# Optimization experiments

Hardware: AMD Instinct MI355X
Metric: run time of the kernel (lower is better)

Reference implementation:

```python
import jax, jax.numpy as jnp
import numpy as np
from jax import lax

B, IMG = 2, 512
FMC, HID, A, NC = 1024, 512, 9, 21
RED, POOL, TOP, IOU_THR = 16, 7, 20, 0.3
NEG = -1e30
# 3 scales x 3 aspect ratios (w, h)
ANCHOR_WH = np.array([[s * np.sqrt(r), s / np.sqrt(r)] for s in (64.0, 128.0, 256.0) for r in (0.5, 1.0, 2.0)], dtype=np.float32)


def conv(x, w, b, stride, pad):
    y = lax.conv_general_dilated(x, w, (stride, stride), pad, dimension_numbers=('NCHW', 'OIHW', 'NCHW'))
    return y + b[None, :, None, None]


def make_anchors(H, W, stride):
    cy = (jnp.arange(H, dtype=jnp.float32) + 0.5) * stride
    cx = (jnp.arange(W, dtype=jnp.float32) + 0.5) * stride
    cyg, cxg = jnp.meshgrid(cy, cx, indexing='ij')  # [H,W]
    wh = jnp.asarray(ANCHOR_WH)  # [A,2]
    w2 = wh[None, None, :, 0] / 2
    h2 = wh[None, None, :, 1] / 2
    cxg = cxg[:, :, None]
    cyg = cyg[:, :, None]
    boxes = jnp.stack([cxg - w2, cyg - h2, cxg + w2, cyg + h2], axis=-1)  # [H,W,A,4]
    return boxes.reshape(-1, 4)


def box_iou(b, boxes):
    # b [4], boxes [N,4], (x1,y1,x2,y2)
    ix1 = jnp.maximum(b[0], boxes[:, 0])
    iy1 = jnp.maximum(b[1], boxes[:, 1])
    ix2 = jnp.minimum(b[2], boxes[:, 2])
    iy2 = jnp.minimum(b[3], boxes[:, 3])
    inter = jnp.maximum(ix2 - ix1, 0.0) * jnp.maximum(iy2 - iy1, 0.0)
    ab = jnp.maximum(b[2] - b[0], 0.0) * jnp.maximum(b[3] - b[1], 0.0)
    ar = jnp.maximum(boxes[:, 2] - boxes[:, 0], 0.0) * jnp.maximum(boxes[:, 3] - boxes[:, 1], 0.0)
    return inter / (ab + ar - inter + 1e-8)


def nms_one(boxes, scores):
    # greedy NMS, fixed TOP selections
    n = scores.shape[0]
    idxs = jnp.arange(n)

    def step(s, _):
        i = jnp.argmax(s)
        b, sc = boxes[i], s[i]
        s = jnp.where((box_iou(b, boxes) > IOU_THR) | (idxs == i), NEG, s)
        return s, (b, sc)

    _, (bs, ss) = lax.scan(step, scores, None, length=TOP)
    return bs, ss  # [TOP,4], [TOP]


def roi_align_one(fm_b, boxes):
    # fm_b [C,H,W], boxes [R,4] in image coords -> [R,C,POOL,POOL]
    C, H, W = fm_b.shape
    b = boxes / RED
    t = (jnp.arange(POOL, dtype=jnp.float32) + 0.5) / POOL
    xs = b[:, 0:1] + jnp.maximum(b[:, 2] - b[:, 0], 0.0)[:, None] * t[None]  # [R,P]
    ys = b[:, 1:2] + jnp.maximum(b[:, 3] - b[:, 1], 0.0)[:, None] * t[None]
    x = jnp.clip(xs[:, None, :], 0.0, W - 1.0) * jnp.ones((1, POOL, 1), jnp.float32)  # [R,P,P]
    y = jnp.clip(ys[:, :, None], 0.0, H - 1.0) * jnp.ones((1, 1, POOL), jnp.float32)
    x0f, y0f = jnp.floor(x), jnp.floor(y)
    x0, y0 = x0f.astype(jnp.int32), y0f.astype(jnp.int32)
    x1 = jnp.minimum(x0 + 1, W - 1)
    y1 = jnp.minimum(y0 + 1, H - 1)
    lx, ly = x - x0f, y - y0f
    v00 = fm_b[:, y0, x0]
    v01 = fm_b[:, y0, x1]
    v10 = fm_b[:, y1, x0]
    v11 = fm_b[:, y1, x1]  # [C,R,P,P]
    out = v00 * (1 - ly) * (1 - lx) + v01 * (1 - ly) * lx + v10 * ly * (1 - lx) + v11 * ly * lx
    return out.transpose(1, 0, 2, 3)


def setup_inputs() -> dict:
    key = jax.random.key(0)
    ks = jax.random.split(key, 16)
    s = 0.02
    return {
        'img': jax.random.normal(ks[0], (B, 3, IMG, IMG), jnp.float32),
        'img_id': jnp.arange(B, dtype=jnp.int32),
        'cnn_w': jax.random.normal(ks[1], (FMC, 3, RED, RED), jnp.float32) * s,
        'cnn_b': jnp.zeros((FMC,), jnp.float32),
        'rpn_w': jax.random.normal(ks[2], (HID, FMC, 3, 3), jnp.float32) * s,
        'rpn_b': jnp.zeros((HID,), jnp.float32),
        'rpn_reg_w': jax.random.normal(ks[3], (A * 4, HID, 1, 1), jnp.float32) * s,
        'rpn_reg_b': jnp.zeros((A * 4,), jnp.float32),
        'rpn_cls_w': jax.random.normal(ks[4], (A, HID, 1, 1), jnp.float32) * s,
        'rpn_cls_b': jnp.zeros((A,), jnp.float32),
        'fc_w': jax.random.normal(ks[5], (FMC * POOL * POOL, 1024), jnp.float32) * 0.005,
        'fc_b': jnp.zeros((1024,), jnp.float32),
        'reg_w': jax.random.normal(ks[6], (1024, 4), jnp.float32) * s,
        'reg_b': jnp.zeros((4,), jnp.float32),
        'cls_w': jax.random.normal(ks[7], (1024, NC), jnp.float32) * s,
        'cls_b': jnp.zeros((NC,), jnp.float32),
    }


def reference(img, img_id, cnn_w, cnn_b, rpn_w, rpn_b, rpn_reg_w, rpn_reg_b, rpn_cls_w, rpn_cls_b, fc_w, fc_b, reg_w, reg_b, cls_w, cls_b):
    fm = jax.nn.relu(conv(img, cnn_w, cnn_b, RED, 'VALID'))  # [B,1024,32,32]
    Bn, C, H, W = fm.shape
    # sliding-window(3x3, stride 1) + per-slice RPN == 3x3 SAME conv + 1x1 heads
    h = jax.nn.relu(conv(fm, rpn_w, rpn_b, 1, 'SAME'))
    rpn_reg = conv(h, rpn_reg_w, rpn_reg_b, 1, 'SAME').transpose(0, 2, 3, 1).reshape(Bn, -1, 4)  # (h,w,a) order
    rpn_cls = conv(h, rpn_cls_w, rpn_cls_b, 1, 'SAME').transpose(0, 2, 3, 1).reshape(Bn, -1)
    anchors = make_anchors(H, W, RED)  # [H*W*A,4]
    nms_reg, nms_cls = jax.vmap(nms_one)(rpn_reg + anchors[None], rpn_cls)  # [B,TOP,4],[B,TOP]
    pooled = jax.vmap(roi_align_one)(fm[img_id], nms_reg)  # [B,TOP,C,P,P]
    flat = pooled.reshape(Bn * TOP, -1)
    hf = jax.nn.relu(flat @ fc_w + fc_b)
    rcnn_reg = (hf @ reg_w + reg_b).reshape(Bn, -1, 4)
    rcnn_cls = (hf @ cls_w + cls_b).reshape(Bn, TOP, -1)
    return rpn_reg, rpn_cls, nms_reg, nms_cls, rcnn_reg, rcnn_cls, anchors
```

## Files before the change

### kernel.cpp

```cpp
#include <hip/hip_runtime.h>
#include <math.h>


#define NEGV (-1e30f)

typedef unsigned short u16;
typedef float v4f __attribute__((ext_vector_type(4)));
typedef short short8 __attribute__((ext_vector_type(8)));

#define O_RPN_REG 0
#define O_RPN_CLS 73728
#define O_NMS_REG 92160
#define O_NMS_CLS 92320
#define O_RCNN_REG 92360
#define O_RCNN_CLS 92520
#define O_ANCH 93360

#define W_FM   0u
#define W_H    2097152u
#define W_PROP 3145728u
#define W_SCR  3219456u
#define W_FLAT 3237888u
#define W_HF   5244928u
#define W_A1H  5285888u
#define W_A1L  6072320u
#define W_B1H  6858752u
#define W_B1L  7251968u
#define W_FMH  7645184u
#define W_FML  8693760u
#define W_B2H  9742336u
#define W_B2L  12101632u
#define W_PART 14460928u

static __device__ __forceinline__ float relu_(float v) { return fmaxf(v, 0.0f); }

static __device__ __forceinline__ u16 bf16_rtne(float x) {
    unsigned int u = __float_as_uint(x);
    unsigned int r = u + 0x7fffu + ((u >> 16) & 1u);
    return (u16)(r >> 16);
}
static __device__ __forceinline__ void split2(float x, u16& h, u16& l) {
    h = bf16_rtne(x);
    const float hf = __uint_as_float(((unsigned int)h) << 16);
    l = bf16_rtne(x - hf);
}
static __device__ __forceinline__ void split8_store(const float* v, u16* dsth, u16* dstl) {
    uint4 H, Lo;
    u16 h0, l0, h1, l1;
    split2(v[0], h0, l0); split2(v[1], h1, l1);
    H.x = (unsigned)h0 | ((unsigned)h1 << 16); Lo.x = (unsigned)l0 | ((unsigned)l1 << 16);
    split2(v[2], h0, l0); split2(v[3], h1, l1);
    H.y = (unsigned)h0 | ((unsigned)h1 << 16); Lo.y = (unsigned)l0 | ((unsigned)l1 << 16);
    split2(v[4], h0, l0); split2(v[5], h1, l1);
    H.z = (unsigned)h0 | ((unsigned)h1 << 16); Lo.z = (unsigned)l0 | ((unsigned)l1 << 16);
    split2(v[6], h0, l0); split2(v[7], h1, l1);
    H.w = (unsigned)h0 | ((unsigned)h1 << 16); Lo.w = (unsigned)l0 | ((unsigned)l1 << 16);
    *(uint4*)dsth = H; *(uint4*)dstl = Lo;
}

static __device__ __forceinline__ void anchor_wh(int a, float& w2, float& h2) {
    double s = (a < 3) ? 64.0 : (a < 6) ? 128.0 : 256.0;
    int rm = a - (a / 3) * 3;
    double r = (rm == 0) ? 0.5 : (rm == 1) ? 1.0 : 2.0;
    double sq = sqrt(r);
    w2 = (float)(s * sq) * 0.5f;
    h2 = (float)(s / sq) * 0.5f;
}

__global__ void k_prep_a1(const float* __restrict__ img, u16* __restrict__ a1h, u16* __restrict__ a1l) {
    const int idx = blockIdx.x * 256 + threadIdx.x;
    const int m = idx / 192, kq = (idx - m * 192) * 4;
    const int b = m >> 10, i = (m >> 5) & 31, j = m & 31;
    const int c = kq >> 8, rem = kq & 255, y = rem >> 4, x = rem & 15;
    const float4 v = *(const float4*)(img + ((size_t)((b * 3 + c) * 512 + i * 16 + y)) * 512 + j * 16 + x);
    ushort4 H, Lo;
    split2(v.x, H.x, Lo.x); split2(v.y, H.y, Lo.y);
    split2(v.z, H.z, Lo.z); split2(v.w, H.w, Lo.w);
    *(ushort4*)(a1h + (size_t)idx * 4) = H;
    *(ushort4*)(a1l + (size_t)idx * 4) = Lo;
}

__global__ void k_split4(const float* __restrict__ src, u16* __restrict__ h, u16* __restrict__ l, int n4) {
    const int idx = blockIdx.x * 256 + threadIdx.x;
    if (idx >= n4) return;
    const float4 v = *(const float4*)(src + (size_t)idx * 4);
    ushort4 H, Lo;
    split2(v.x, H.x, Lo.x); split2(v.y, H.y, Lo.y);
    split2(v.z, H.z, Lo.z); split2(v.w, H.w, Lo.w);
    *(ushort4*)(h + (size_t)idx * 4) = H;
    *(ushort4*)(l + (size_t)idx * 4) = Lo;
}

__global__ void k_prep_w2(const float* __restrict__ w, u16* __restrict__ bh, u16* __restrict__ bl) {
    const int idx = blockIdx.x * 256 + threadIdx.x;
    const int oc = idx / 2304, r = idx - oc * 2304, d = r >> 8, ic4 = (r & 255) * 4;
    const float* p = w + (size_t)oc * 9216 + (size_t)ic4 * 9 + d;
    float4 v; v.x = p[0]; v.y = p[9]; v.z = p[18]; v.w = p[27];
    ushort4 H, Lo;
    split2(v.x, H.x, Lo.x); split2(v.y, H.y, Lo.y);
    split2(v.z, H.z, Lo.z); split2(v.w, H.w, Lo.w);
    const size_t o = (size_t)oc * 9216 + d * 1024 + ic4;
    *(ushort4*)(bh + o) = H;
    *(ushort4*)(bl + o) = Lo;
}

template<int MODE>
__global__ __launch_bounds__(256, 1) void k_gemm(
        const u16* __restrict__ Agh, const u16* __restrict__ Agl,
        const u16* __restrict__ Bgh, const u16* __restrict__ Bgl,
        const float* __restrict__ bias, float* __restrict__ Cout,
        const int KA, const int KB, const int nchunk, const int ldc, const int do_bias_relu,
        u16* __restrict__ outH, u16* __restrict__ outL) {
    __shared__ __align__(16) u16 AsH[128 * 32];
    __shared__ __align__(16) u16 AsL[128 * 32];
    __shared__ __align__(16) u16 BsH[64 * 32];
    __shared__ __align__(16) u16 BsL[64 * 32];
    const int tid = threadIdx.x;
    const int w = tid >> 6, L = tid & 63;
    const int q = L >> 4, lr = L & 15;
    const int wm = w >> 1, wn = w & 1;
    const int m0 = blockIdx.x * 128, n0 = blockIdx.y * 64;
    const int icoff = blockIdx.z * 512;
    float* C = Cout + (MODE == 1 ? (size_t)blockIdx.z * (2048u * 512u) : (size_t)0);
    const int seg = L & 3, rsub = L >> 2;

    u16* ldst[6];
    const u16* gbase[6];
    int arow_b[6], arow_i[6], arow_j[6];
    int kindv[6];
#pragma unroll
    for (int s = 0; s < 6; ++s) {
        const int idx = w * 6 + s;
        int kind, inst;
        if (idx < 8)       { kind = 0; inst = idx; }
        else if (idx < 16) { kind = 1; inst = idx - 8; }
        else if (idx < 20) { kind = 2; inst = idx - 16; }
        else               { kind = 3; inst = idx - 20; }
        kindv[s] = kind;
        const int r = inst * 16 + rsub;
        u16* lb = (kind == 0) ? AsH : (kind == 1) ? AsL : (kind == 2) ? BsH : BsL;
        ldst[s] = lb + r * 32 + seg * 8;
        arow_b[s] = 0; arow_i[s] = 0; arow_j[s] = 0;
        if (kind >= 2) {
            const u16* gb = (kind == 2) ? Bgh : Bgl;
            gbase[s] = gb + (size_t)(n0 + r) * KB + seg * 8;
        } else if (MODE == 0) {
            const u16* gb = (kind == 0) ? Agh : Agl;
            gbase[s] = gb + (size_t)(m0 + r) * KA + seg * 8;
        } else {
            const int m = m0 + r;
            arow_b[s] = m >> 10; arow_i[s] = (m >> 5) & 31; arow_j[s] = m & 31;
            gbase[s] = (kind == 0) ? Agh : Agl;
        }
    }

    v4f acc[4][2];
#pragma unroll
    for (int t = 0; t < 4; ++t)
#pragma unroll
        for (int u2 = 0; u2 < 2; ++u2) acc[t][u2] = (v4f){0.f, 0.f, 0.f, 0.f};

    uint4 ubuf[6];
    bool okbuf[6];

#define LOAD6(c_) do { \
    int d_, ic_, kB_; \
    if (MODE == 0) { kB_ = (c_) * 32; d_ = 0; ic_ = kB_; } \
    else { d_ = (c_) >> 4; ic_ = icoff + ((c_) & 15) * 32; kB_ = d_ * 1024 + ic_; } \
    const int di_ = d_ / 3, dj_ = d_ - di_ * 3; \
    _Pragma("unroll") \
    for (int s = 0; s < 6; ++s) { \
        if (kindv[s] >= 2) { ubuf[s] = *(const uint4*)(gbase[s] + kB_); okbuf[s] = true; } \
        else if (MODE == 0) { ubuf[s] = *(const uint4*)(gbase[s] + ic_); okbuf[s] = true; } \
        else { \
            const int y_ = arow_i[s] + di_ - 1, x_ = arow_j[s] + dj_ - 1; \
            const bool ok_ = ((unsigned)y_ < 32u) && ((unsigned)x_ < 32u); \
            const int yc_ = ok_ ? y_ : 0, xc_ = ok_ ? x_ : 0; \
            ubuf[s] = *(const uint4*)(gbase[s] + (size_t)(((arow_b[s] * 32 + yc_) * 32 + xc_)) * 1024 + ic_ + seg * 8); \
            okbuf[s] = ok_; \
        } \
    } \
} while (0)

    LOAD6(0);
    for (int c = 0; c < nchunk; ++c) {
        __syncthreads();
#pragma unroll
        for (int s = 0; s < 6; ++s) {
            uint4 v = ubuf[s];
            if (MODE == 1 && !okbuf[s]) { v.x = 0u; v.y = 0u; v.z = 0u; v.w = 0u; }
            *(uint4*)ldst[s] = v;
        }
        __syncthreads();
        if (c + 1 < nchunk) LOAD6(c + 1);
        short8 ah[4], al[4], bh[2], bl[2];
#pragma unroll
        for (int t = 0; t < 4; ++t) {
            ah[t] = *(const short8*)(AsH + (wm * 64 + t * 16 + lr) * 32 + q * 8);
            al[t] = *(const short8*)(AsL + (wm * 64 + t * 16 + lr) * 32 + q * 8);
        }
#pragma unroll
        for (int u2 = 0; u2 < 2; ++u2) {
            bh[u2] = *(const short8*)(BsH + (wn * 32 + u2 * 16 + lr) * 32 + q * 8);
            bl[u2] = *(const short8*)(BsL + (wn * 32 + u2 * 16 + lr) * 32 + q * 8);
        }
#pragma unroll
        for (int t = 0; t < 4; ++t)
#pragma unroll
            for (int u2 = 0; u2 < 2; ++u2) {
                acc[t][u2] = __builtin_amdgcn_mfma_f32_16x16x32_bf16(ah[t], bh[u2], acc[t][u2], 0, 0, 0);
                acc[t][u2] = __builtin_amdgcn_mfma_f32_16x16x32_bf16(ah[t], bl[u2], acc[t][u2], 0, 0, 0);
                acc[t][u2] = __builtin_amdgcn_mfma_f32_16x16x32_bf16(al[t], bh[u2], acc[t][u2], 0, 0, 0);
            }
    }
#undef LOAD6

#pragma unroll
    for (int t = 0; t < 4; ++t) {
        const int row = m0 + wm * 64 + t * 16 + q * 4;
#pragma unroll
        for (int u2 = 0; u2 < 2; ++u2) {
            const int col = n0 + wn * 32 + u2 * 16 + lr;
            const float bv = do_bias_relu ? bias[col] : 0.f;
#pragma unroll
            for (int r = 0; r < 4; ++r) {
                float vv = acc[t][u2][r];
                if (do_bias_relu) vv = relu_(vv + bv);
                C[(size_t)(row + r) * ldc + col] = vv;
                if (MODE == 0 && outH != nullptr) {
                    u16 hh, ll; split2(vv, hh, ll);
                    outH[(size_t)(row + r) * 1024 + col] = hh;
                    outL[(size_t)(row + r) * 1024 + col] = ll;
                }
            }
        }
    }
}

__global__ __launch_bounds__(64) void k_rpn_heads(const float* __restrict__ part,
        const float* __restrict__ rpnb,
        const float* __restrict__ regw, const float* __restrict__ regb,
        const float* __restrict__ clsw, const float* __restrict__ clsb,
        float* __restrict__ out, float* __restrict__ prop, float* __restrict__ scr) {
    __shared__ __align__(16) float hrow[512];
    const int m = blockIdx.x, tid = threadIdx.x;
    const int b = m >> 10, qd = m & 1023, ii = qd >> 5, jj = qd & 31;
    for (int i = tid * 4; i < 512; i += 256) {
        const float4 p0 = *(const float4*)(part + (size_t)m * 512 + i);
        const float4 p1 = *(const float4*)(part + (size_t)(2048 * 512) + (size_t)m * 512 + i);
        const float4 bb = *(const float4*)(rpnb + i);
        float4 o;
        o.x = relu_(p0.x + p1.x + bb.x); o.y = relu_(p0.y + p1.y + bb.y);
        o.z = relu_(p0.z + p1.z + bb.z); o.w = relu_(p0.w + p1.w + bb.w);
        *(float4*)&hrow[i] = o;
    }
    __syncthreads();
    if (tid < 45) {
        const int isreg = (tid < 36);
        const float* wp = isreg ? (regw + (size_t)tid * 512) : (clsw + (size_t)(tid - 36) * 512);
        float acc2 = isreg ? regb[tid] : clsb[tid - 36];
        for (int k = 0; k < 512; k += 4) {
            const float4 wv = *(const float4*)(wp + k);
            acc2 += hrow[k + 0] * wv.x; acc2 += hrow[k + 1] * wv.y;
            acc2 += hrow[k + 2] * wv.z; acc2 += hrow[k + 3] * wv.w;
        }
        if (isreg) {
            out[O_RPN_REG + (size_t)b * 36864 + qd * 36 + tid] = acc2;
            const int a = tid >> 2, cc = tid & 3;
            float w2, h2; anchor_wh(a, w2, h2);
            const float cx = ((float)jj + 0.5f) * 16.f, cy = ((float)ii + 0.5f) * 16.f;
            const float av = (cc == 0) ? cx - w2 : (cc == 1) ? cy - h2 : (cc == 2) ? cx + w2 : cy + h2;
            prop[(size_t)b * 36864 + qd * 36 + tid] = acc2 + av;
        } else {
            const int n = tid - 36;
            out[O_RPN_CLS + (size_t)b * 9216 + qd * 9 + n] = acc2;
            scr[(size_t)b * 9216 + qd * 9 + n] = acc2;
        }
    }
    if (b == 0 && tid >= 48 && tid < 57) {
        const int a = tid - 48;
        float w2, h2; anchor_wh(a, w2, h2);
        const float cx = ((float)jj + 0.5f) * 16.f, cy = ((float)ii + 0.5f) * 16.f;
        const float4 av4 = make_float4(cx - w2, cy - h2, cx + w2, cy + h2);
        *(float4*)(out + O_ANCH + (size_t)(qd * 9 + a) * 4) = av4;
    }
}

__global__ __launch_bounds__(512) void k_nms3(const float* __restrict__ prop,
        const float* __restrict__ scr, float* __restrict__ out) {
    __shared__ float wv_[2][8];
    __shared__ int wi_[2][8];
    const int b = blockIdx.x, tid = threadIdx.x;
    const int lane = tid & 63, wid = tid >> 6;
    const float* P = prop + (size_t)b * 36864;
    float4 bx[18]; float sv[18];
#pragma unroll
    for (int k = 0; k < 18; ++k) {
        const int i = tid * 18 + k;
        bx[k] = *(const float4*)(P + (size_t)i * 4);
        sv[k] = scr[b * 9216 + i];
    }
    for (int t = 0; t < 20; ++t) {
        float bv = -3.4e38f; int bi = 0;
#pragma unroll
        for (int k = 0; k < 18; ++k)
            if (sv[k] > bv) { bv = sv[k]; bi = tid * 18 + k; }
#pragma unroll
        for (int off = 1; off < 64; off <<= 1) {
            const float ov = __shfl_xor(bv, off);
            const int oi = __shfl_xor(bi, off);
            if (ov > bv || (ov == bv && oi < bi)) { bv = ov; bi = oi; }
        }
        if (lane == 0) { wv_[t & 1][wid] = bv; wi_[t & 1][wid] = bi; }
        __syncthreads();
        float rb = wv_[t & 1][0]; int sel = wi_[t & 1][0];
#pragma unroll
        for (int j = 1; j < 8; ++j) {
            const float v2 = wv_[t & 1][j]; const int i2 = wi_[t & 1][j];
            if (v2 > rb || (v2 == rb && i2 < sel)) { rb = v2; sel = i2; }
        }
        const float4 bb = *(const float4*)(P + (size_t)sel * 4);
        if (tid == 0) {
            *(float4*)(out + O_NMS_REG + (size_t)(b * 20 + t) * 4) = bb;
            out[O_NMS_CLS + b * 20 + t] = rb;
        }
        const float ab2 = fmaxf(bb.z - bb.x, 0.f) * fmaxf(bb.w - bb.y, 0.f);
#pragma unroll
        for (int k = 0; k < 18; ++k) {
            const float ix1 = fmaxf(bb.x, bx[k].x), iy1 = fmaxf(bb.y, bx[k].y);
            const float ix2 = fminf(bb.z, bx[k].z), iy2 = fminf(bb.w, bx[k].w);
            const float inter = fmaxf(ix2 - ix1, 0.f) * fmaxf(iy2 - iy1, 0.f);
            const float ar2 = fmaxf(bx[k].z - bx[k].x, 0.f) * fmaxf(bx[k].w - bx[k].y, 0.f);
            const float iou = inter / (ab2 + ar2 - inter + 1e-8f);
            if (iou > 0.3f || (tid * 18 + k) == sel) sv[k] = NEGV;
        }
    }
}

__global__ __launch_bounds__(256) void k_roi(const float* __restrict__ fm,
        const int* __restrict__ img_id, const float* __restrict__ nreg,
        float* __restrict__ flat) {
    const int py = blockIdx.x, roi = blockIdx.y, b = blockIdx.z;
    const float* bx = nreg + (size_t)(b * 20 + roi) * 4;
    const float b0 = bx[0] * 0.0625f, b1 = bx[1] * 0.0625f;
    const float b2 = bx[2] * 0.0625f, b3 = bx[3] * 0.0625f;
    const float wd = fmaxf(b2 - b0, 0.f), hg = fmaxf(b3 - b1, 0.f);
    const float tyv = ((float)py + 0.5f) / 7.0f;
    const float ycv = fminf(fmaxf(b1 + hg * tyv, 0.f), 31.f);
    const float y0f = floorf(ycv);
    const int y0 = (int)y0f, y1 = min(y0 + 1, 31);
    const float ly = ycv - y0f, omly = 1.f - ly;
    const int bb = img_id[b];
    const float* fmb = fm + (size_t)bb * (32 * 32 * 1024);
    const size_t orow = (size_t)(b * 20 + roi) * 50176 + (size_t)py * 7;
    for (int px = 0; px < 7; ++px) {
        const float txv = ((float)px + 0.5f) / 7.0f;
        const float xcv = fminf(fmaxf(b0 + wd * txv, 0.f), 31.f);
        const float x0f = floorf(xcv);
        const int x0 = (int)x0f, x1 = min(x0 + 1, 31);
        const float lx = xcv - x0f, omlx = 1.f - lx;
        const int o00 = ((y0 * 32) + x0) << 10, o01 = ((y0 * 32) + x1) << 10;
        const int o10 = ((y1 * 32) + x0) << 10, o11 = ((y1 * 32) + x1) << 10;
        for (int u = 0; u < 4; ++u) {
            const int c = threadIdx.x + u * 256;
            const float v00 = fmb[o00 + c], v01 = fmb[o01 + c];
            const float v10 = fmb[o10 + c], v11 = fmb[o11 + c];
            const float val = ((v00 * omly) * omlx) + ((v01 * omly) * lx)
                            + ((v10 * ly) * omlx) + ((v11 * ly) * lx);
            flat[orow + (size_t)c * 49 + px] = val;
        }
    }
}

__global__ void k_hf_init(const float* __restrict__ fcb, float* __restrict__ hf) {
    const int i = blockIdx.x * 256 + threadIdx.x;
    if (i < 40 * 1024) hf[i] = fcb[i & 1023];
}

__global__ __launch_bounds__(256, 2) void k_fc_mfma(const float* __restrict__ flat,
        const float* __restrict__ fcw, float* __restrict__ hf) {
    __shared__ __align__(16) u16 AsH[4 * 48 * 8];
    __shared__ __align__(16) u16 AsL[4 * 48 * 8];
    __shared__ __align__(16) u16 BsH[4 * 256 * 8];
    __shared__ __align__(16) u16 BsL[4 * 256 * 8];
    const int tid = threadIdx.x;
    const int w = tid >> 6, L = tid & 63, q = L >> 4, lr = L & 15;
    const int n0 = blockIdx.x * 256, kb = blockIdx.y * 512;
    if (tid < 32) {
        const int oct = tid >> 3, m = 40 + (tid & 7);
        *(uint4*)(AsH + (oct * 48 + m) * 8) = make_uint4(0, 0, 0, 0);
        *(uint4*)(AsL + (oct * 48 + m) * 8) = make_uint4(0, 0, 0, 0);
    }
    const int am = tid >> 2, aoct = tid & 3;
    const float* abase = flat + (size_t)am * 50176 + kb + aoct * 8;
    const float* bcol = fcw + n0 + tid;

    v4f acc[3][4];
#pragma unroll
    for (int mt = 0; mt < 3; ++mt)
#pragma unroll
        for (int nt = 0; nt < 4; ++nt) acc[mt][nt] = (v4f){0.f, 0.f, 0.f, 0.f};

    float areg[8];
    float breg[4][8];

#define LOADF(c_) do { \
    if (tid < 160) { \
        const float4 u_ = *(const float4*)(abase + (c_) * 32); \
        const float4 v_ = *(const float4*)(abase + (c_) * 32 + 4); \
        areg[0] = u_.x; areg[1] = u_.y; areg[2] = u_.z; areg[3] = u_.w; \
        areg[4] = v_.x; areg[5] = v_.y; areg[6] = v_.z; areg[7] = v_.w; \
    } \
    _Pragma("unroll") \
    for (int o_ = 0; o_ < 4; ++o_) \
        _Pragma("unroll") \
        for (int j_ = 0; j_ < 8; ++j_) \
            breg[o_][j_] = bcol[(size_t)(kb + (c_) * 32 + o_ * 8 + j_) * 1024]; \
} while (0)

    LOADF(0);
    for (int c = 0; c < 16; ++c) {
        __syncthreads();
        if (tid < 160)
            split8_store(areg, AsH + (aoct * 48 + am) * 8, AsL + (aoct * 48 + am) * 8);
#pragma unroll
        for (int o = 0; o < 4; ++o)
            split8_store(breg[o], BsH + (o * 256 + tid) * 8, BsL + (o * 256 + tid) * 8);
        __syncthreads();
        if (c + 1 < 16) LOADF(c + 1);
        short8 ah[3], al[3], bh2[4], bl2[4];
#pragma unroll
        for (int mt = 0; mt < 3; ++mt) {
            ah[mt] = *(const short8*)(AsH + (q * 48 + mt * 16 + lr) * 8);
            al[mt] = *(const short8*)(AsL + (q * 48 + mt * 16 + lr) * 8);
        }
#pragma unroll
        for (int nt = 0; nt < 4; ++nt) {
            bh2[nt] = *(const short8*)(BsH + (q * 256 + w * 64 + nt * 16 + lr) * 8);
            bl2[nt] = *(const short8*)(BsL + (q * 256 + w * 64 + nt * 16 + lr) * 8);
        }
#pragma unroll
        for (int mt = 0; mt < 3; ++mt)
#pragma unroll
            for (int nt = 0; nt < 4; ++nt) {
                acc[mt][nt] = __builtin_amdgcn_mfma_f32_16x16x32_bf16(ah[mt], bh2[nt], acc[mt][nt], 0, 0, 0);
                acc[mt][nt] = __builtin_amdgcn_mfma_f32_16x16x32_bf16(ah[mt], bl2[nt], acc[mt][nt], 0, 0, 0);
                acc[mt][nt] = __builtin_amdgcn_mfma_f32_16x16x32_bf16(al[mt], bh2[nt], acc[mt][nt], 0, 0, 0);
            }
    }
#undef LOADF

#pragma unroll
    for (int mt = 0; mt < 3; ++mt) {
#pragma unroll
        for (int nt = 0; nt < 4; ++nt) {
#pragma unroll
            for (int r = 0; r < 4; ++r) {
                const int row = mt * 16 + q * 4 + r;
                if (row < 40)
                    atomicAdd(hf + (size_t)row * 1024 + n0 + w * 64 + nt * 16 + lr, acc[mt][nt][r]);
            }
        }
    }
}

__global__ __launch_bounds__(64) void k_heads(const float* __restrict__ hf,
        const float* __restrict__ regw, const float* __restrict__ regb,
        const float* __restrict__ clsw, const float* __restrict__ clsb,
        float* __restrict__ out) {
    __shared__ __align__(16) float hrow[1024];
    const int m = blockIdx.x, tid = threadIdx.x;
    for (int i = tid * 4; i < 1024; i += 256) {
        const float4 v = *(const float4*)(hf + (size_t)m * 1024 + i);
        hrow[i + 0] = relu_(v.x); hrow[i + 1] = relu_(v.y);
        hrow[i + 2] = relu_(v.z); hrow[i + 3] = relu_(v.w);
    }
    __syncthreads();
    if (tid < 25) {
        float acc2 = 0.f;
        if (tid < 4) {
            for (int k = 0; k < 1024; ++k) acc2 += hrow[k] * regw[(size_t)k * 4 + tid];
            out[O_RCNN_REG + m * 4 + tid] = acc2 + regb[tid];
        } else {
            const int n = tid - 4;
            for (int k = 0; k < 1024; ++k) acc2 += hrow[k] * clsw[(size_t)k * 21 + n];
            out[O_RCNN_CLS + m * 21 + n] = acc2 + clsb[n];
        }
    }
}

extern "C" void kernel_launch(void* const* d_in, const int* in_sizes, int n_in,
                              void* d_out, int out_size, void* d_ws, size_t ws_size,
                              hipStream_t stream) {
    (void)in_sizes; (void)n_in; (void)out_size; (void)ws_size;
    const float* img       = (const float*)d_in[0];
    const int*   img_id    = (const int*)  d_in[1];
    const float* cnn_w     = (const float*)d_in[2];
    const float* cnn_b     = (const float*)d_in[3];
    const float* rpn_w     = (const float*)d_in[4];
    const float* rpn_b     = (const float*)d_in[5];
    const float* rpn_reg_w = (const float*)d_in[6];
    const float* rpn_reg_b = (const float*)d_in[7];
    const float* rpn_cls_w = (const float*)d_in[8];
    const float* rpn_cls_b = (const float*)d_in[9];
    const float* fc_w      = (const float*)d_in[10];
    const float* fc_b      = (const float*)d_in[11];
    const float* reg_w     = (const float*)d_in[12];
    const float* reg_b     = (const float*)d_in[13];
    const float* cls_w     = (const float*)d_in[14];
    const float* cls_b     = (const float*)d_in[15];
    float* out = (float*)d_out;
    float* ws  = (float*)d_ws;

    float* fm   = ws + W_FM;
    float* prop = ws + W_PROP;
    float* scr  = ws + W_SCR;
    float* flat = ws + W_FLAT;
    float* hf   = ws + W_HF;
    u16* a1h = (u16*)(ws + W_A1H);
    u16* a1l = (u16*)(ws + W_A1L);
    u16* b1h = (u16*)(ws + W_B1H);
    u16* b1l = (u16*)(ws + W_B1L);
    u16* fmh = (u16*)(ws + W_FMH);
    u16* fml = (u16*)(ws + W_FML);
    u16* b2h = (u16*)(ws + W_B2H);
    u16* b2l = (u16*)(ws + W_B2L);
    float* part = ws + W_PART;

    k_prep_a1<<<1536, 256, 0, stream>>>(img, a1h, a1l);
    k_split4<<<768, 256, 0, stream>>>(cnn_w, b1h, b1l, 196608);
    k_prep_w2<<<4608, 256, 0, stream>>>(rpn_w, b2h, b2l);
    k_gemm<0><<<dim3(16, 16, 1), 256, 0, stream>>>(a1h, a1l, b1h, b1l, cnn_b, fm,
                                                   768, 768, 24, 1024, 1, fmh, fml);
    k_gemm<1><<<dim3(16, 8, 2), 256, 0, stream>>>(fmh, fml, b2h, b2l, nullptr, part,
                                                  1024, 9216, 144, 512, 0, nullptr, nullptr);
    k_rpn_heads<<<2048, 64, 0, stream>>>(part, rpn_b, rpn_reg_w, rpn_reg_b, rpn_cls_w, rpn_cls_b,
                                         out, prop, scr);
    k_nms3<<<2, 512, 0, stream>>>(prop, scr, out);
    k_roi<<<dim3(7, 20, 2), 256, 0, stream>>>(fm, img_id, out + O_NMS_REG, flat);
    k_hf_init<<<160, 256, 0, stream>>>(fc_b, hf);
    k_fc_mfma<<<dim3(4, 98), 256, 0, stream>>>(flat, fc_w, hf);
    k_heads<<<40, 64, 0, stream>>>(hf, reg_w, reg_b, cls_w, cls_b, out);
}
```

Baseline: 672.0 us.

## Double-buffer GEMM LDS via direct global-to-LDS loads and raise split-K to six

The bf16x3 GEMM kernel now loads tiles straight from global memory into double-buffered LDS using global_load_lds, dropping the register staging and one barrier per chunk so that loads overlap with MFMA work. Out-of-bounds conv taps read from a small zeroed buffer instead of being masked in registers. The RPN 3x3 conv GEMM grid's split-K grows from 2 to 6 slices (256 to 768 blocks) with launch_bounds raised to allow 3 blocks per CU, and the head kernel now sums six partials. The cost is twice the LDS per block, more partial-sum traffic, and reuse of the flat workspace region for partials before the ROI stage overwrites it.

```diff
diff --git a/kernel.cpp b/kernel.cpp
--- a/kernel.cpp
+++ b/kernel.cpp
@@ -17,7 +17,7 @@
 #define O_ANCH 93360
 
 #define W_FM   0u
-#define W_H    2097152u
+#define W_ZERO 2097152u
 #define W_PROP 3145728u
 #define W_SCR  3219456u
 #define W_FLAT 3237888u
@@ -34,6 +34,12 @@
 
 static __device__ __forceinline__ float relu_(float v) { return fmaxf(v, 0.0f); }
 
+static __device__ __forceinline__ void gload16(const void* g, void* l) {
+    __builtin_amdgcn_global_load_lds(
+        (const __attribute__((address_space(1))) unsigned int*)g,
+        (__attribute__((address_space(3))) unsigned int*)l, 16, 0, 0);
+}
+
 static __device__ __forceinline__ u16 bf16_rtne(float x) {
     unsigned int u = __float_as_uint(x);
     unsigned int r = u + 0x7fffu + ((u >> 16) & 1u);
@@ -67,7 +73,9 @@
     h2 = (float)(s / sq) * 0.5f;
 }
 
-__global__ void k_prep_a1(const float* __restrict__ img, u16* __restrict__ a1h, u16* __restrict__ a1l) {
+__global__ void k_prep_a1(const float* __restrict__ img, u16* __restrict__ a1h, u16* __restrict__ a1l,
+                          float* __restrict__ zbuf) {
+    if (blockIdx.x == 0 && threadIdx.x < 64) zbuf[threadIdx.x] = 0.0f;
     const int idx = blockIdx.x * 256 + threadIdx.x;
     const int m = idx / 192, kq = (idx - m * 192) * 4;
     const int b = m >> 10, i = (m >> 5) & 31, j = m & 31;
@@ -105,26 +113,33 @@
 }
 
 template<int MODE>
-__global__ __launch_bounds__(256, 1) void k_gemm(
+__global__ __launch_bounds__(256, 3) void k_gemm(
         const u16* __restrict__ Agh, const u16* __restrict__ Agl,
         const u16* __restrict__ Bgh, const u16* __restrict__ Bgl,
-        const float* __restrict__ bias, float* __restrict__ Cout,
+        const float* __restrict__ bias, float* __restrict__ Cout, float* __restrict__ Cout2,
         const int KA, const int KB, const int nchunk, const int ldc, const int do_bias_relu,
-        u16* __restrict__ outH, u16* __restrict__ outL) {
-    __shared__ __align__(16) u16 AsH[128 * 32];
-    __shared__ __align__(16) u16 AsL[128 * 32];
-    __shared__ __align__(16) u16 BsH[64 * 32];
-    __shared__ __align__(16) u16 BsL[64 * 32];
+        u16* __restrict__ outH, u16* __restrict__ outL, const float* __restrict__ zbuf) {
+    __shared__ __align__(16) u16 AsH[2 * 128 * 32];
+    __shared__ __align__(16) u16 AsL[2 * 128 * 32];
+    __shared__ __align__(16) u16 BsH[2 * 64 * 32];
+    __shared__ __align__(16) u16 BsL[2 * 64 * 32];
     const int tid = threadIdx.x;
     const int w = tid >> 6, L = tid & 63;
     const int q = L >> 4, lr = L & 15;
     const int wm = w >> 1, wn = w & 1;
     const int m0 = blockIdx.x * 128, n0 = blockIdx.y * 64;
-    const int icoff = blockIdx.z * 512;
-    float* C = Cout + (MODE == 1 ? (size_t)blockIdx.z * (2048u * 512u) : (size_t)0);
+    const int zbase = blockIdx.z * nchunk;
+    float* C;
+    if (MODE == 1) {
+        C = (blockIdx.z < 4) ? (Cout + (size_t)blockIdx.z * (2048u * 512u))
+                             : (Cout2 + (size_t)(blockIdx.z - 4) * (2048u * 512u));
+    } else {
+        C = Cout;
+    }
     const int seg = L & 3, rsub = L >> 2;
 
-    u16* ldst[6];
+    u16* lseg[6];
+    int lsz[6];
     const u16* gbase[6];
     int arow_b[6], arow_i[6], arow_j[6];
     int kindv[6];
@@ -139,7 +154,8 @@
         kindv[s] = kind;
         const int r = inst * 16 + rsub;
         u16* lb = (kind == 0) ? AsH : (kind == 1) ? AsL : (kind == 2) ? BsH : BsL;
-        ldst[s] = lb + r * 32 + seg * 8;
+        lseg[s] = lb + r * 32 + seg * 8;
+        lsz[s] = (kind < 2) ? (128 * 32) : (64 * 32);
         arow_b[s] = 0; arow_i[s] = 0; arow_j[s] = 0;
         if (kind >= 2) {
             const u16* gb = (kind == 2) ? Bgh : Bgl;
@@ -160,49 +176,43 @@
 #pragma unroll
         for (int u2 = 0; u2 < 2; ++u2) acc[t][u2] = (v4f){0.f, 0.f, 0.f, 0.f};
 
-    uint4 ubuf[6];
-    bool okbuf[6];
-
-#define LOAD6(c_) do { \
+#define ISSUE(c_, bb_) do { \
     int d_, ic_, kB_; \
     if (MODE == 0) { kB_ = (c_) * 32; d_ = 0; ic_ = kB_; } \
-    else { d_ = (c_) >> 4; ic_ = icoff + ((c_) & 15) * 32; kB_ = d_ * 1024 + ic_; } \
+    else { const int g_ = zbase + (c_); d_ = g_ >> 5; ic_ = (g_ & 31) << 5; kB_ = d_ * 1024 + ic_; } \
     const int di_ = d_ / 3, dj_ = d_ - di_ * 3; \
     _Pragma("unroll") \
     for (int s = 0; s < 6; ++s) { \
-        if (kindv[s] >= 2) { ubuf[s] = *(const uint4*)(gbase[s] + kB_); okbuf[s] = true; } \
-        else if (MODE == 0) { ubuf[s] = *(const uint4*)(gbase[s] + ic_); okbuf[s] = true; } \
+        const u16* gsrc_; \
+        if (kindv[s] >= 2) gsrc_ = gbase[s] + kB_; \
+        else if (MODE == 0) gsrc_ = gbase[s] + ic_; \
         else { \
             const int y_ = arow_i[s] + di_ - 1, x_ = arow_j[s] + dj_ - 1; \
             const bool ok_ = ((unsigned)y_ < 32u) && ((unsigned)x_ < 32u); \
             const int yc_ = ok_ ? y_ : 0, xc_ = ok_ ? x_ : 0; \
-            ubuf[s] = *(const uint4*)(gbase[s] + (size_t)(((arow_b[s] * 32 + yc_) * 32 + xc_)) * 1024 + ic_ + seg * 8); \
-            okbuf[s] = ok_; \
+            const u16* ga_ = gbase[s] + (size_t)((arow_b[s] * 32 + yc_) * 32 + xc_) * 1024 + ic_ + seg * 8; \
+            gsrc_ = ok_ ? ga_ : (const u16*)zbuf; \
         } \
+        gload16(gsrc_, lseg[s] + (bb_) * lsz[s]); \
     } \
 } while (0)
 
-    LOAD6(0);
+    int cur = 0;
+    ISSUE(0, 0);
     for (int c = 0; c < nchunk; ++c) {
         __syncthreads();
-#pragma unroll
-        for (int s = 0; s < 6; ++s) {
-            uint4 v = ubuf[s];
-            if (MODE == 1 && !okbuf[s]) { v.x = 0u; v.y = 0u; v.z = 0u; v.w = 0u; }
-            *(uint4*)ldst[s] = v;
-        }
-        __syncthreads();
-        if (c + 1 < nchunk) LOAD6(c + 1);
+        if (c + 1 < nchunk) ISSUE(c + 1, cur ^ 1);
+        const int ao = cur * (128 * 32), bo = cur * (64 * 32);
         short8 ah[4], al[4], bh[2], bl[2];
 #pragma unroll
         for (int t = 0; t < 4; ++t) {
-            ah[t] = *(const short8*)(AsH + (wm * 64 + t * 16 + lr) * 32 + q * 8);
-            al[t] = *(const short8*)(AsL + (wm * 64 + t * 16 + lr) * 32 + q * 8);
+            ah[t] = *(const short8*)(AsH + ao + (wm * 64 + t * 16 + lr) * 32 + q * 8);
+            al[t] = *(const short8*)(AsL + ao + (wm * 64 + t * 16 + lr) * 32 + q * 8);
         }
 #pragma unroll
         for (int u2 = 0; u2 < 2; ++u2) {
-            bh[u2] = *(const short8*)(BsH + (wn * 32 + u2 * 16 + lr) * 32 + q * 8);
-            bl[u2] = *(const short8*)(BsL + (wn * 32 + u2 * 16 + lr) * 32 + q * 8);
+            bh[u2] = *(const short8*)(BsH + bo + (wn * 32 + u2 * 16 + lr) * 32 + q * 8);
+            bl[u2] = *(const short8*)(BsL + bo + (wn * 32 + u2 * 16 + lr) * 32 + q * 8);
         }
 #pragma unroll
         for (int t = 0; t < 4; ++t)
@@ -212,8 +222,9 @@
                 acc[t][u2] = __builtin_amdgcn_mfma_f32_16x16x32_bf16(ah[t], bl[u2], acc[t][u2], 0, 0, 0);
                 acc[t][u2] = __builtin_amdgcn_mfma_f32_16x16x32_bf16(al[t], bh[u2], acc[t][u2], 0, 0, 0);
             }
-    }
-#undef LOAD6
+        cur ^= 1;
+    }
+#undef ISSUE
 
 #pragma unroll
     for (int t = 0; t < 4; ++t) {
@@ -237,7 +248,8 @@
     }
 }
 
-__global__ __launch_bounds__(64) void k_rpn_heads(const float* __restrict__ part,
+__global__ __launch_bounds__(64) void k_rpn_heads(const float* __restrict__ partA,
+        const float* __restrict__ partB,
         const float* __restrict__ rpnb,
         const float* __restrict__ regw, const float* __restrict__ regb,
         const float* __restrict__ clsw, const float* __restrict__ clsb,
@@ -246,12 +258,19 @@
     const int m = blockIdx.x, tid = threadIdx.x;
     const int b = m >> 10, qd = m & 1023, ii = qd >> 5, jj = qd & 31;
     for (int i = tid * 4; i < 512; i += 256) {
-        const float4 p0 = *(const float4*)(part + (size_t)m * 512 + i);
-        const float4 p1 = *(const float4*)(part + (size_t)(2048 * 512) + (size_t)m * 512 + i);
+        const size_t ro = (size_t)m * 512 + i;
+        const float4 a0 = *(const float4*)(partA + ro);
+        const float4 a1 = *(const float4*)(partA + 1048576u + ro);
+        const float4 a2 = *(const float4*)(partA + 2097152u + ro);
+        const float4 a3 = *(const float4*)(partA + 3145728u + ro);
+        const float4 a4 = *(const float4*)(partB + ro);
+        const float4 a5 = *(const float4*)(partB + 1048576u + ro);
         const float4 bb = *(const float4*)(rpnb + i);
         float4 o;
-        o.x = relu_(p0.x + p1.x + bb.x); o.y = relu_(p0.y + p1.y + bb.y);
-        o.z = relu_(p0.z + p1.z + bb.z); o.w = relu_(p0.w + p1.w + bb.w);
+        o.x = relu_(a0.x + a1.x + a2.x + a3.x + a4.x + a5.x + bb.x);
+        o.y = relu_(a0.y + a1.y + a2.y + a3.y + a4.y + a5.y + bb.y);
+        o.z = relu_(a0.z + a1.z + a2.z + a3.z + a4.z + a5.z + bb.z);
+        o.w = relu_(a0.w + a1.w + a2.w + a3.w + a4.w + a5.w + bb.w);
         *(float4*)&hrow[i] = o;
     }
     __syncthreads();
@@ -513,6 +532,7 @@
     float* ws  = (float*)d_ws;
 
     float* fm   = ws + W_FM;
+    float* zbuf = ws + W_ZERO;
     float* prop = ws + W_PROP;
     float* scr  = ws + W_SCR;
     float* flat = ws + W_FLAT;
@@ -525,16 +545,17 @@
     u16* fml = (u16*)(ws + W_FML);
     u16* b2h = (u16*)(ws + W_B2H);
     u16* b2l = (u16*)(ws + W_B2L);
-    float* part = ws + W_PART;
-
-    k_prep_a1<<<1536, 256, 0, stream>>>(img, a1h, a1l);
+    float* partA = ws + W_FLAT;
+    float* partB = ws + W_PART;
+
+    k_prep_a1<<<1536, 256, 0, stream>>>(img, a1h, a1l, zbuf);
     k_split4<<<768, 256, 0, stream>>>(cnn_w, b1h, b1l, 196608);
     k_prep_w2<<<4608, 256, 0, stream>>>(rpn_w, b2h, b2l);
-    k_gemm<0><<<dim3(16, 16, 1), 256, 0, stream>>>(a1h, a1l, b1h, b1l, cnn_b, fm,
-                                                   768, 768, 24, 1024, 1, fmh, fml);
-    k_gemm<1><<<dim3(16, 8, 2), 256, 0, stream>>>(fmh, fml, b2h, b2l, nullptr, part,
-                                                  1024, 9216, 144, 512, 0, nullptr, nullptr);
-    k_rpn_heads<<<2048, 64, 0, stream>>>(part, rpn_b, rpn_reg_w, rpn_reg_b, rpn_cls_w, rpn_cls_b,
+    k_gemm<0><<<dim3(16, 16, 1), 256, 0, stream>>>(a1h, a1l, b1h, b1l, cnn_b, fm, nullptr,
+                                                   768, 768, 24, 1024, 1, fmh, fml, zbuf);
+    k_gemm<1><<<dim3(16, 8, 6), 256, 0, stream>>>(fmh, fml, b2h, b2l, nullptr, partA, partB,
+                                                  1024, 9216, 48, 512, 0, nullptr, nullptr, zbuf);
+    k_rpn_heads<<<2048, 64, 0, stream>>>(partA, partB, rpn_b, rpn_reg_w, rpn_reg_b, rpn_cls_w, rpn_cls_b,
                                          out, prop, scr);
     k_nms3<<<2, 512, 0, stream>>>(prop, scr, out);
     k_roi<<<dim3(7, 20, 2), 256, 0, stream>>>(fm, img_id, out + O_NMS_REG, flat);
```

Measured after the change: 623.1 us. 7.3% less time.
